# Optimization experiments

Measured on AMD Instinct MI355X. Metric: run time of the kernel, lower is better.

Reference implementation:

```python
import jax, jax.numpy as jnp
import numpy as np

RADIUS = 0.1
NSAMPLE = 64


def ball_query(xyz, new_xyz, pointsnum, radius, nsample):
    """xyz (B,N,2), new_xyz (B,S,2), pointsnum (B,) -> idx (B,S,nsample) int32.
    Mirrors CUDA ball_query: for each query take the first `nsample` point
    indices (in index order) whose squared distance < radius^2 and index <
    pointsnum[b]; slots beyond the number found are padded with the first
    found index (0 if none found)."""
    N = xyz.shape[1]
    # (B,S,N) squared distances
    d2 = jnp.sum((new_xyz[:, :, None, :] - xyz[:, None, :, :]) ** 2, axis=-1)
    valid = jnp.arange(N, dtype=jnp.int32)[None, None, :] < pointsnum[:, None, None]
    mask = (d2 < radius * radius) & valid
    # key = point index if in ball else N (sentinel); smallest `nsample` keys
    key = jnp.where(mask, jnp.arange(N, dtype=jnp.int32), N)
    neg_small, _ = jax.lax.top_k(-key, nsample)          # largest of -key == smallest keys
    sorted_keys = -neg_small                              # ascending in-ball indices, N-padded
    first = sorted_keys[..., :1]
    pad = jnp.where(first < N, first, 0)
    idx = jnp.where(sorted_keys < N, sorted_keys, pad)
    return idx.astype(jnp.int32)


def group(features, idx):
    """features (B,C,N), idx (B,S,K) -> (B,C,S,K)."""
    return jax.vmap(lambda f, i: f[:, i])(features, idx)


def setup_inputs() -> dict:
    key = jax.random.key(0)
    k1, k2, k3 = jax.random.split(key, 3)
    B, N, S, C = 4, 16384, 2048, 64
    xyz = jax.random.uniform(k1, (B, N, 2), dtype=jnp.float32)
    new_xyz = jax.random.uniform(k2, (B, S, 2), dtype=jnp.float32)
    features = jax.random.normal(k3, (B, C, N), dtype=jnp.float32)
    pointsnum = jnp.full((B,), N, dtype=jnp.int32)
    return {"xyz": xyz, "new_xyz": new_xyz, "features": features, "pointsnum": pointsnum}


def reference(xyz, new_xyz, features, pointsnum):
    # QueryAndGroup(radius=RADIUS, nsample=NSAMPLE, use_xyz=True)
    idx = ball_query(xyz, new_xyz, pointsnum, RADIUS, NSAMPLE)  # (B,S,K) int32
    xyz_t = jnp.transpose(xyz, (0, 2, 1))                        # (B,2,N)
    grouped_xyz = group(xyz_t, idx)                              # (B,2,S,K)
    grouped_xyz = grouped_xyz - jnp.transpose(new_xyz, (0, 2, 1))[..., None]
    grouped_features = group(features, idx)                      # (B,C,S,K)
    new_features = jnp.concatenate([grouped_xyz, grouped_features], axis=1)  # (B,2+C,S,K)
    return new_features
```

## Files before the change

kernel.cpp:

```cpp
#include <hip/hip_runtime.h>
#include <stdint.h>

#define B 4
#define N 16384
#define S 2048
#define C 64
#define K 64
#define OC 66
#define R2 0.01f
#define NXCD 8
#define TP 1089

typedef float f32x4 __attribute__((ext_vector_type(4)));

__global__ __launch_bounds__(256) void transpose_kernel(const float* __restrict__ f,
                                                        float* __restrict__ ft) {
    __shared__ float tile[64 * 65];
    const int n0 = blockIdx.x * 64;
    const int b  = blockIdx.y;
    const int t  = threadIdx.x;

    const int nl = t & 63, cl = t >> 6;
    #pragma unroll
    for (int cc = cl; cc < 64; cc += 4) {
        tile[cc * 65 + nl] = __builtin_nontemporal_load(&f[((size_t)b * C + cc) * N + n0 + nl]);
    }
    __syncthreads();

    const int cl2 = t & 63, nl2 = t >> 6;
    #pragma unroll
    for (int nn = nl2; nn < 64; nn += 4) {
        ft[((size_t)b * N + n0 + nn) * C + cl2] = tile[cl2 * 65 + nn];
    }
}

__global__ __launch_bounds__(256) void qag2_kernel(const float* __restrict__ xyz,
                                                   const float* __restrict__ new_xyz,
                                                   const float* __restrict__ ft,
                                                   const int* __restrict__ pointsnum,
                                                   float* __restrict__ out) {
    __shared__ int   s_idx[4][K];
    __shared__ float tile[4 * TP];

    const int t    = threadIdx.x;
    const int lane = t & 63;
    const int wu   = __builtin_amdgcn_readfirstlane(t >> 6);

    const int nwg = (B * S) / 4;
    const int bid = blockIdx.x;
    const int swz = (bid & (NXCD - 1)) * (nwg / NXCD) + (bid >> 3);

    const int q0 = swz * 4;
    const int b  = q0 >> 11;
    const int s0 = q0 & (S - 1);
    const int q  = q0 + wu;
    const int s  = s0 + wu;

    const float qx = new_xyz[(size_t)q * 2 + 0];
    const float qy = new_xyz[(size_t)q * 2 + 1];
    const float* __restrict__ xb = xyz + (size_t)b * N * 2;

    int pn = pointsnum[b];
    pn = pn < 0 ? 0 : (pn > N ? N : pn);
    int cnt = 0;
    for (int base = 0; base < pn && cnt < K; base += 256) {
        float2 p[4];
        #pragma unroll
        for (int u = 0; u < 4; ++u) {
            int i  = base + u * 64 + lane;
            int ic = i < N ? i : N - 1;
            p[u] = *(const float2*)&xb[(size_t)ic * 2];
        }
        #pragma unroll
        for (int u = 0; u < 4; ++u) {
            const int i = base + u * 64 + lane;
            bool ok = false;
            if (i < pn) {
                const float dx = __fsub_rn(qx, p[u].x);
                const float dy = __fsub_rn(qy, p[u].y);
                const float d2 = __fadd_rn(__fmul_rn(dx, dx), __fmul_rn(dy, dy));
                ok = d2 < R2;
            }
            const unsigned long long m = __ballot(ok);
            if (ok) {
                const int pos = cnt + __popcll(m & ((1ull << lane) - 1ull));
                if (pos < K) s_idx[wu][pos] = i;
            }
            cnt += __popcll(m);
        }
    }
    const int found = cnt < K ? cnt : K;
    const int first = (found > 0) ? s_idx[wu][0] : 0;
    const int id    = (lane < found) ? s_idx[wu][lane] : first;
    s_idx[wu][lane] = id;

    const size_t SK = (size_t)S * K;
    const float2 pxy = *(const float2*)&xb[(size_t)id * 2];
    {
        float* ob = out + ((size_t)b * OC) * SK + (size_t)s * K;
        ob[lane]      = pxy.x - qx;
        ob[SK + lane] = pxy.y - qy;
    }

    const int kk = lane >> 2;
    const int c2 = lane & 3;
    const int ql = lane >> 4;
    const int m  = lane & 15;
    const float* __restrict__ ftb = ft + (size_t)b * N * C;

    #pragma unroll
    for (int cc = 0; cc < 4; ++cc) {
        f32x4 v[4];
        #pragma unroll
        for (int g = 0; g < 4; ++g) {
            const int p  = g * 16 + kk;
            const int ip = s_idx[wu][p];
            v[g] = *(const f32x4*)&ftb[(size_t)ip * C + cc * 16 + c2 * 4];
        }

        __syncthreads();
        #pragma unroll
        for (int g = 0; g < 4; ++g) {
            const int p = g * 16 + kk;
            *(f32x4*)&tile[wu * TP + p * 17 + c2 * 4] = v[g];
        }
        __syncthreads();

        #pragma unroll
        for (int j = 0; j < 4; ++j) {
            const int cw = 4 * wu + j;
            f32x4 vv;
            vv.x = tile[ql * TP + (4 * m + 0) * 17 + cw];
            vv.y = tile[ql * TP + (4 * m + 1) * 17 + cw];
            vv.z = tile[ql * TP + (4 * m + 2) * 17 + cw];
            vv.w = tile[ql * TP + (4 * m + 3) * 17 + cw];
            float* bp = out + ((size_t)b * OC + 2 + cc * 16 + cw) * SK + (size_t)s0 * K;
            *(((f32x4*)bp) + lane) = vv;
        }
    }
}

__global__ __launch_bounds__(256) void qag_fallback(const float* __restrict__ xyz,
                                                    const float* __restrict__ new_xyz,
                                                    const float* __restrict__ feat,
                                                    const int* __restrict__ pointsnum,
                                                    float* __restrict__ out) {
    __shared__ int s_idx[4][K];

    const int t    = threadIdx.x;
    const int lane = t & 63;
    const int wu   = __builtin_amdgcn_readfirstlane(t >> 6);
    const int q0   = blockIdx.x * 4;
    const int b    = q0 >> 11;
    const int q    = q0 + wu;
    const int s    = (q0 & (S - 1)) + wu;

    const float qx = new_xyz[(size_t)q * 2 + 0];
    const float qy = new_xyz[(size_t)q * 2 + 1];
    const float* __restrict__ xb = xyz + (size_t)b * N * 2;

    int pn = pointsnum[b];
    pn = pn < 0 ? 0 : (pn > N ? N : pn);
    int cnt = 0;
    for (int base = 0; base < pn && cnt < K; base += 256) {
        float2 p[4];
        #pragma unroll
        for (int u = 0; u < 4; ++u) {
            int i  = base + u * 64 + lane;
            int ic = i < N ? i : N - 1;
            p[u] = *(const float2*)&xb[(size_t)ic * 2];
        }
        #pragma unroll
        for (int u = 0; u < 4; ++u) {
            const int i = base + u * 64 + lane;
            bool ok = false;
            if (i < pn) {
                const float dx = __fsub_rn(qx, p[u].x);
                const float dy = __fsub_rn(qy, p[u].y);
                const float d2 = __fadd_rn(__fmul_rn(dx, dx), __fmul_rn(dy, dy));
                ok = d2 < R2;
            }
            const unsigned long long mm = __ballot(ok);
            if (ok) {
                const int pos = cnt + __popcll(mm & ((1ull << lane) - 1ull));
                if (pos < K) s_idx[wu][pos] = i;
            }
            cnt += __popcll(mm);
        }
    }
    const int found = cnt < K ? cnt : K;
    const int first = (found > 0) ? s_idx[wu][0] : 0;
    const int id    = (lane < found) ? s_idx[wu][lane] : first;

    const size_t SK = (size_t)S * K;
    const float2 pxy = *(const float2*)&xb[(size_t)id * 2];
    float* ob = out + ((size_t)b * OC) * SK + (size_t)s * K;
    ob[lane]      = pxy.x - qx;
    ob[SK + lane] = pxy.y - qy;

    const float* __restrict__ fb = feat + (size_t)b * C * N;
    for (int c = 0; c < C; ++c) {
        ob[(size_t)(2 + c) * SK + lane] = fb[(size_t)c * N + id];
    }
}

extern "C" void kernel_launch(void* const* d_in, const int* in_sizes, int n_in,
                              void* d_out, int out_size, void* d_ws, size_t ws_size,
                              hipStream_t stream) {
    const float* xyz       = (const float*)d_in[0];
    const float* new_xyz   = (const float*)d_in[1];
    const float* feat      = (const float*)d_in[2];
    const int*   pointsnum = (const int*)d_in[3];
    float*       out       = (float*)d_out;

    const size_t ft_bytes = (size_t)B * N * C * sizeof(float);
    if (ws_size >= ft_bytes) {
        float* ft = (float*)d_ws;
        transpose_kernel<<<dim3(N / 64, B), 256, 0, stream>>>(feat, ft);
        qag2_kernel<<<B * S / 4, 256, 0, stream>>>(xyz, new_xyz, ft, pointsnum, out);
    } else {
        qag_fallback<<<B * S / 4, 256, 0, stream>>>(xyz, new_xyz, feat, pointsnum, out);
    }
}
```

Baseline: 52.27 us.

## Prefetch next point batch in ball query and make feature transpose per-wave

The ball-query scan now double-buffers point coordinates, loading the next 256 points while the current batch is tested, to hide global-load latency. The feature gather/transpose through LDS is now private to each wave: each wave writes its own tile and stores 16 channels of 64 floats (256 B rows) per query, removing the two block-wide barriers per channel chunk. The cost is narrower stores (per-lane scalar rather than f32x4 across four queries), one extra speculative load batch past the early exit, and a lane-strided LDS read pattern (stride 17) that may cause bank conflicts.

```diff
diff --git a/kernel.cpp b/kernel.cpp
--- a/kernel.cpp
+++ b/kernel.cpp
@@ -34,7 +34,7 @@
     }
 }
 
-__global__ __launch_bounds__(256) void qag2_kernel(const float* __restrict__ xyz,
+__global__ __launch_bounds__(256) void qag3_kernel(const float* __restrict__ xyz,
                                                    const float* __restrict__ new_xyz,
                                                    const float* __restrict__ ft,
                                                    const int* __restrict__ pointsnum,
@@ -52,9 +52,8 @@
 
     const int q0 = swz * 4;
     const int b  = q0 >> 11;
-    const int s0 = q0 & (S - 1);
     const int q  = q0 + wu;
-    const int s  = s0 + wu;
+    const int s  = (q0 & (S - 1)) + wu;
 
     const float qx = new_xyz[(size_t)q * 2 + 0];
     const float qy = new_xyz[(size_t)q * 2 + 1];
@@ -63,13 +62,19 @@
     int pn = pointsnum[b];
     pn = pn < 0 ? 0 : (pn > N ? N : pn);
     int cnt = 0;
+    float2 p[4], pf[4];
+    #pragma unroll
+    for (int u = 0; u < 4; ++u) {
+        const int i  = u * 64 + lane;
+        const int ic = i < N ? i : N - 1;
+        p[u] = *(const float2*)&xb[(size_t)ic * 2];
+    }
     for (int base = 0; base < pn && cnt < K; base += 256) {
-        float2 p[4];
-        #pragma unroll
-        for (int u = 0; u < 4; ++u) {
-            int i  = base + u * 64 + lane;
-            int ic = i < N ? i : N - 1;
-            p[u] = *(const float2*)&xb[(size_t)ic * 2];
+        #pragma unroll
+        for (int u = 0; u < 4; ++u) {
+            const int i  = base + 256 + u * 64 + lane;
+            const int ic = i < N ? i : N - 1;
+            pf[u] = *(const float2*)&xb[(size_t)ic * 2];
         }
         #pragma unroll
         for (int u = 0; u < 4; ++u) {
@@ -88,6 +93,8 @@
             }
             cnt += __popcll(m);
         }
+        #pragma unroll
+        for (int u = 0; u < 4; ++u) p[u] = pf[u];
     }
     const int found = cnt < K ? cnt : K;
     const int first = (found > 0) ? s_idx[wu][0] : 0;
@@ -96,46 +103,33 @@
 
     const size_t SK = (size_t)S * K;
     const float2 pxy = *(const float2*)&xb[(size_t)id * 2];
-    {
-        float* ob = out + ((size_t)b * OC) * SK + (size_t)s * K;
-        ob[lane]      = pxy.x - qx;
-        ob[SK + lane] = pxy.y - qy;
-    }
+    float* ob = out + ((size_t)b * OC) * SK + (size_t)s * K;
+    ob[lane]      = pxy.x - qx;
+    ob[SK + lane] = pxy.y - qy;
 
     const int kk = lane >> 2;
     const int c2 = lane & 3;
-    const int ql = lane >> 4;
-    const int m  = lane & 15;
     const float* __restrict__ ftb = ft + (size_t)b * N * C;
+    float* owt = tile + wu * TP;
 
     #pragma unroll
     for (int cc = 0; cc < 4; ++cc) {
         f32x4 v[4];
         #pragma unroll
         for (int g = 0; g < 4; ++g) {
-            const int p  = g * 16 + kk;
-            const int ip = s_idx[wu][p];
+            const int pt = g * 16 + kk;
+            const int ip = s_idx[wu][pt];
             v[g] = *(const f32x4*)&ftb[(size_t)ip * C + cc * 16 + c2 * 4];
         }
-
-        __syncthreads();
         #pragma unroll
         for (int g = 0; g < 4; ++g) {
-            const int p = g * 16 + kk;
-            *(f32x4*)&tile[wu * TP + p * 17 + c2 * 4] = v[g];
-        }
-        __syncthreads();
-
-        #pragma unroll
-        for (int j = 0; j < 4; ++j) {
-            const int cw = 4 * wu + j;
-            f32x4 vv;
-            vv.x = tile[ql * TP + (4 * m + 0) * 17 + cw];
-            vv.y = tile[ql * TP + (4 * m + 1) * 17 + cw];
-            vv.z = tile[ql * TP + (4 * m + 2) * 17 + cw];
-            vv.w = tile[ql * TP + (4 * m + 3) * 17 + cw];
-            float* bp = out + ((size_t)b * OC + 2 + cc * 16 + cw) * SK + (size_t)s0 * K;
-            *(((f32x4*)bp) + lane) = vv;
+            const int pt = g * 16 + kk;
+            *(f32x4*)&owt[pt * 17 + c2 * 4] = v[g];
+        }
+        #pragma unroll
+        for (int c = 0; c < 16; ++c) {
+            const float vv = owt[lane * 17 + c];
+            ob[(size_t)(2 + cc * 16 + c) * SK + lane] = vv;
         }
     }
 }
@@ -217,7 +211,7 @@
     if (ws_size >= ft_bytes) {
         float* ft = (float*)d_ws;
         transpose_kernel<<<dim3(N / 64, B), 256, 0, stream>>>(feat, ft);
-        qag2_kernel<<<B * S / 4, 256, 0, stream>>>(xyz, new_xyz, ft, pointsnum, out);
+        qag3_kernel<<<B * S / 4, 256, 0, stream>>>(xyz, new_xyz, ft, pointsnum, out);
     } else {
         qag_fallback<<<B * S / 4, 256, 0, stream>>>(xyz, new_xyz, feat, pointsnum, out);
     }
```

Result: faster. 48.66 us, median of 2 (-6.9%).
